# Optimization experiments

Hardware: AMD Instinct MI355X
Metric: run time of the kernel (lower is better)

Reference implementation:

```python
import jax, jax.numpy as jnp
import numpy as np

EPS = 1e-3  # keras LayerNormalization default epsilon

def layernorm(x, gamma, beta):
    mu = jnp.mean(x, axis=-1, keepdims=True)
    var = jnp.var(x, axis=-1, keepdims=True)
    return (x - mu) * jax.lax.rsqrt(var + EPS) * gamma + beta

def setup_inputs() -> dict:
    key = jax.random.key(0)
    ks = jax.random.split(key, 20)
    B, N, T, Dimg, H = 512, 100, 14, 2048, 768
    s = lambda k, *sh: jax.random.normal(k, sh, dtype=jnp.float32) * 0.02
    return {
        "img_feat": jax.random.normal(ks[0], (B, N, Dimg), dtype=jnp.float32),
        "ques_feat": jax.random.normal(ks[1], (B, T, H), dtype=jnp.float32),
        "Wc": s(ks[2], Dimg, H), "bc": jnp.zeros((H,), jnp.float32),
        "Wq": s(ks[3], H, H),    "bq": jnp.zeros((H,), jnp.float32),
        "Wi": s(ks[4], Dimg, H), "bi": jnp.zeros((H,), jnp.float32),
        "wqa": s(ks[5], H, 1), "bqa": jnp.zeros((1,), jnp.float32),
        "wia": s(ks[6], H, 1), "bia": jnp.zeros((1,), jnp.float32),
        "g1": jnp.ones((N,), jnp.float32), "b1": jnp.zeros((N,), jnp.float32),
        "g2": jnp.ones((H,), jnp.float32), "b2": jnp.zeros((H,), jnp.float32),
        "g3": jnp.ones((T,), jnp.float32), "b3": jnp.zeros((T,), jnp.float32),
        "g4": jnp.ones((H,), jnp.float32), "b4": jnp.zeros((H,), jnp.float32),
        "g5": jnp.ones((N,), jnp.float32), "b5": jnp.zeros((N,), jnp.float32),
    }

def reference(img_feat, ques_feat, Wc, bc, Wq, bq, Wi, bi, wqa, bqa, wia, bia,
              g1, b1, g2, b2, g3, b3, g4, b4, g5, b5):
    # img_feat: [B,N,Dimg], ques_feat: [B,T,H]
    img_corr = img_feat @ Wc + bc                                   # [B,N,H]
    wm = jnp.einsum('bth,bnh->btn', ques_feat, img_corr)            # [B,T,N]
    wm = jax.nn.relu(layernorm(wm, g1, b1))
    ques_embed = ques_feat @ Wq + bq                                # [B,T,H]
    img_embed = img_feat @ Wi + bi                                  # [B,N,H]
    transform_img = jnp.einsum('btn,bnh->bth', wm, img_embed)       # [B,T,H]
    ques_atten_sum = jax.nn.relu(layernorm(transform_img + ques_embed, g2, b2))
    # dropout is identity at inference
    ques_atten = (ques_atten_sum @ wqa + bqa)[..., 0]               # [B,T]
    ques_atten = jax.nn.softmax(layernorm(ques_atten, g3, b3), axis=-1)
    transform_ques = jnp.einsum('btn,bth->bnh', wm, ques_embed)     # [B,N,H]
    img_atten_sum = jax.nn.relu(layernorm(transform_ques + img_embed, g4, b4))
    img_atten = (img_atten_sum @ wia + bia)[..., 0]                 # [B,N]
    img_atten = jax.nn.softmax(layernorm(img_atten, g5, b5), axis=-1)
    ques_atten_feat = jnp.einsum('bt,bth->bh', ques_atten, ques_feat)  # [B,H]
    img_atten_feat = jnp.einsum('bn,bnd->bd', img_atten, img_feat)     # [B,Dimg]
    return (img_atten_feat, ques_atten_feat)
```

## Files before the change

### kernel.cpp

```cpp
#include <hip/hip_runtime.h>

using f32x4     = __attribute__((ext_vector_type(4))) float;
using bf16x8    = __attribute__((ext_vector_type(8))) short;
using ushort4_t = __attribute__((ext_vector_type(4))) unsigned short;
using ushort8_t = __attribute__((ext_vector_type(8))) unsigned short;
using uint4_t   = __attribute__((ext_vector_type(4))) unsigned int;

__device__ __forceinline__ unsigned short f2bf(float f) {
    unsigned u = __builtin_bit_cast(unsigned, f);
    u += 0x7fffu + ((u >> 16) & 1u);
    return (unsigned short)(u >> 16);
}
__device__ __forceinline__ float bf2f(unsigned short h) {
    return __builtin_bit_cast(float, (unsigned)h << 16);
}

__device__ __forceinline__ float wave_sum(float v) {
#pragma unroll
    for (int off = 32; off > 0; off >>= 1) v += __shfl_xor(v, off, 64);
    return v;
}
__device__ __forceinline__ float wave_max(float v) {
#pragma unroll
    for (int off = 32; off > 0; off >>= 1) v = fmaxf(v, __shfl_xor(v, off, 64));
    return v;
}

#define GLP(p)  ((const __attribute__((address_space(1))) void*)(p))
#define LDSP(p) ((__attribute__((address_space(3))) void*)(p))

__global__ __launch_bounds__(256) void cvt_bf16(const float* __restrict__ in,
                                                unsigned short* __restrict__ out, long n8) {
    long i = (long)blockIdx.x * 256 + threadIdx.x;
    long stride = (long)gridDim.x * 256;
    for (; i < n8; i += stride) {
        const float4* p = (const float4*)(in + i * 8);
        float4 a = p[0], b = p[1];
        ushort8_t v;
        v[0] = f2bf(a.x); v[1] = f2bf(a.y); v[2] = f2bf(a.z); v[3] = f2bf(a.w);
        v[4] = f2bf(b.x); v[5] = f2bf(b.y); v[6] = f2bf(b.z); v[7] = f2bf(b.w);
        *(ushort8_t*)(out + i * 8) = v;
    }
}

__global__ void pack_w(const float* __restrict__ Wc, const float* __restrict__ Wi,
                       unsigned short* __restrict__ Wp) {
    int n = blockIdx.x, k = blockIdx.y * 256 + threadIdx.x;
    float v = (n < 768) ? Wc[(size_t)k * 768 + n] : Wi[(size_t)k * 768 + (n - 768)];
    Wp[(size_t)n * 2048 + k] = f2bf(v);
}

__global__ void pack_wq(const float* __restrict__ Wq, unsigned short* __restrict__ Wqt) {
    int n = blockIdx.x, k = blockIdx.y * 256 + threadIdx.x;
    Wqt[(size_t)n * 768 + k] = f2bf(Wq[(size_t)k * 768 + n]);
}

template <int OUTBF>
__global__ __launch_bounds__(512, 1) void gemm8(
    const unsigned short* __restrict__ A, const unsigned short* __restrict__ Bt,
    const float* __restrict__ bias0, const float* __restrict__ bias1, int nsplit,
    void* __restrict__ Cv, int N, int K, int NTN)
{
    __shared__ unsigned short LA[4][8192];
    __shared__ unsigned short LB[4][8192];
    const int tid = threadIdx.x, lane = tid & 63, wid = tid >> 6;

    int nwg = (int)gridDim.x, bid = (int)blockIdx.x;
    if ((nwg & 7) == 0) { int cpx = nwg >> 3; bid = (bid & 7) * cpx + (bid >> 3); }
    const int tn = bid % NTN, tm = bid / NTN;
    const size_t m0 = (size_t)tm * 256, n0 = (size_t)tn * 256;
    const int NT = K >> 5;

    const int wr = wid >> 2, wc = wid & 3;
    const int wm = wr * 128, wn = wc * 64;
    const int fr = lane & 15, fs = lane >> 4;

    const int c0 = tid, c1 = tid + 512;
    const int r0 = c0 >> 2, s0 = ((c0 & 3) - (r0 >> 1)) & 3;
    const int r1 = c1 >> 2, s1 = ((c1 & 3) - (r1 >> 1)) & 3;
    const unsigned short* gA0 = A + (m0 + r0) * K + s0 * 8;
    const unsigned short* gA1 = A + (m0 + r1) * K + s1 * 8;
    const unsigned short* gB0 = Bt + (n0 + r0) * K + s0 * 8;
    const unsigned short* gB1 = Bt + (n0 + r1) * K + s1 * 8;

    int offA[8], offB[4];
#pragma unroll
    for (int mf = 0; mf < 8; ++mf) {
        int r = wm + mf * 16 + fr;
        offA[mf] = (4 * r + ((fs + (r >> 1)) & 3)) * 8;
    }
#pragma unroll
    for (int nf = 0; nf < 4; ++nf) {
        int r = wn + nf * 16 + fr;
        offB[nf] = (4 * r + ((fs + (r >> 1)) & 3)) * 8;
    }

    f32x4 acc[8][4];
#pragma unroll
    for (int i = 0; i < 8; ++i)
#pragma unroll
        for (int j = 0; j < 4; ++j) acc[i][j] = (f32x4){0.f, 0.f, 0.f, 0.f};

#pragma unroll
    for (int t = 0; t < 3; ++t) {
        if (t < NT) {
            __builtin_amdgcn_global_load_lds(GLP(gA0 + t * 32), LDSP(&LA[t][c0 * 8]), 16, 0, 0);
            __builtin_amdgcn_global_load_lds(GLP(gA1 + t * 32), LDSP(&LA[t][c1 * 8]), 16, 0, 0);
            __builtin_amdgcn_global_load_lds(GLP(gB0 + t * 32), LDSP(&LB[t][c0 * 8]), 16, 0, 0);
            __builtin_amdgcn_global_load_lds(GLP(gB1 + t * 32), LDSP(&LB[t][c1 * 8]), 16, 0, 0);
        }
    }

    for (int T = 0; T < NT; ++T) {
        const int buf = T & 3, pb = (T + 3) & 3;
        const int rem = NT - 1 - T;
        if (rem >= 2)      asm volatile("s_waitcnt vmcnt(8)" ::: "memory");
        else if (rem == 1) asm volatile("s_waitcnt vmcnt(4)" ::: "memory");
        else               asm volatile("s_waitcnt vmcnt(0)" ::: "memory");
        __builtin_amdgcn_s_barrier();
        __builtin_amdgcn_sched_barrier(0);

        bf16x8 av[4], bv[4];
#pragma unroll
        for (int mf = 0; mf < 4; ++mf) av[mf] = *(const bf16x8*)&LA[buf][offA[mf]];
#pragma unroll
        for (int nf = 0; nf < 4; ++nf) bv[nf] = *(const bf16x8*)&LB[buf][offB[nf]];
        if (T + 3 < NT) {
            __builtin_amdgcn_global_load_lds(GLP(gA0 + (size_t)(T + 3) * 32), LDSP(&LA[pb][c0 * 8]), 16, 0, 0);
            __builtin_amdgcn_global_load_lds(GLP(gA1 + (size_t)(T + 3) * 32), LDSP(&LA[pb][c1 * 8]), 16, 0, 0);
        }
        asm volatile("s_waitcnt lgkmcnt(0)" ::: "memory");
        __builtin_amdgcn_sched_barrier(0);
        __builtin_amdgcn_s_setprio(1);
#pragma unroll
        for (int mf = 0; mf < 4; ++mf)
#pragma unroll
            for (int nf = 0; nf < 4; ++nf)
                acc[mf][nf] = __builtin_amdgcn_mfma_f32_16x16x32_bf16(av[mf], bv[nf], acc[mf][nf], 0, 0, 0);
        __builtin_amdgcn_s_setprio(0);

#pragma unroll
        for (int mf = 0; mf < 4; ++mf) av[mf] = *(const bf16x8*)&LA[buf][offA[4 + mf]];
        if (T + 3 < NT) {
            __builtin_amdgcn_global_load_lds(GLP(gB0 + (size_t)(T + 3) * 32), LDSP(&LB[pb][c0 * 8]), 16, 0, 0);
            __builtin_amdgcn_global_load_lds(GLP(gB1 + (size_t)(T + 3) * 32), LDSP(&LB[pb][c1 * 8]), 16, 0, 0);
        }
        asm volatile("s_waitcnt lgkmcnt(0)" ::: "memory");
        __builtin_amdgcn_sched_barrier(0);
        __builtin_amdgcn_s_setprio(1);
#pragma unroll
        for (int mf = 0; mf < 4; ++mf)
#pragma unroll
            for (int nf = 0; nf < 4; ++nf)
                acc[4 + mf][nf] = __builtin_amdgcn_mfma_f32_16x16x32_bf16(av[mf], bv[nf], acc[4 + mf][nf], 0, 0, 0);
        __builtin_amdgcn_s_setprio(0);
    }

#pragma unroll
    for (int nf = 0; nf < 4; ++nf) {
        int col = (int)n0 + wn + nf * 16 + fr;
        float bs = (col < nsplit) ? bias0[col] : bias1[col - nsplit];
#pragma unroll
        for (int mf = 0; mf < 8; ++mf) {
            size_t rowb = m0 + wm + mf * 16 + fs * 4;
#pragma unroll
            for (int r = 0; r < 4; ++r) {
                float v = acc[mf][nf][r] + bs;
                if (OUTBF) ((unsigned short*)Cv)[(rowb + r) * N + col] = f2bf(v);
                else       ((float*)Cv)[(rowb + r) * N + col] = v;
            }
        }
    }
}

__global__ __launch_bounds__(256) void wm_kernel(
    const unsigned short* __restrict__ qbf, const unsigned short* __restrict__ imgCE,
    const float* __restrict__ g1, const float* __restrict__ b1,
    float* __restrict__ wm_g)
{
    const int b = blockIdx.x, tid = threadIdx.x, lane = tid & 63, wid = tid >> 6;
    __shared__ float qf[14 * 768];
    __shared__ float wmr[14][100];

    const ushort8_t* src = (const ushort8_t*)(qbf + (size_t)b * 14 * 768);
    for (int i = tid; i < 14 * 768 / 8; i += 256) {
        ushort8_t v = src[i];
#pragma unroll
        for (int j = 0; j < 8; ++j) qf[i * 8 + j] = bf2f(v[j]);
    }
    __syncthreads();

    for (int n = wid; n < 100; n += 4) {
        const unsigned short* row = imgCE + ((size_t)b * 100 + n) * 1536;
        float r[12];
#pragma unroll
        for (int j = 0; j < 12; ++j) r[j] = bf2f(row[lane + 64 * j]);
        for (int t = 0; t < 14; ++t) {
            const float* q = qf + t * 768;
            float s = 0.f;
#pragma unroll
            for (int j = 0; j < 12; ++j) s = fmaf(r[j], q[lane + 64 * j], s);
            s = wave_sum(s);
            if (lane == 0) wmr[t][n] = s;
        }
    }
    __syncthreads();

    for (int t = wid; t < 14; t += 4) {
        float x0 = wmr[t][lane];
        float x1 = (lane + 64 < 100) ? wmr[t][lane + 64] : 0.f;
        float s = wave_sum(x0 + x1);
        float q = wave_sum(x0 * x0 + x1 * x1);
        float mu = s * (1.f / 100.f);
        float var = q * (1.f / 100.f) - mu * mu;
        float rs = rsqrtf(var + 1e-3f);
        float* dst = wm_g + ((size_t)b * 14 + t) * 100;
        {
            float v = (x0 - mu) * rs * g1[lane] + b1[lane];
            dst[lane] = v > 0.f ? v : 0.f;
        }
        if (lane + 64 < 100) {
            float v = (x1 - mu) * rs * g1[lane + 64] + b1[lane + 64];
            dst[lane + 64] = v > 0.f ? v : 0.f;
        }
    }
}

__global__ __launch_bounds__(256) void ques_kernel(
    const float* __restrict__ qf_g, const float* __restrict__ qe_g,
    const unsigned short* __restrict__ imgCE, const float* __restrict__ wm_g,
    const float* __restrict__ g2, const float* __restrict__ b2,
    const float* __restrict__ g3, const float* __restrict__ b3,
    const float* __restrict__ wqa, const float* __restrict__ bqa,
    float* __restrict__ out_q)
{
    const int b = blockIdx.x, tid = threadIdx.x, lane = tid & 63, wid = tid >> 6;
    __shared__ float qe[14 * 768];
    __shared__ float wm[14 * 100];
    __shared__ float red[4][28];
    __shared__ float mu_s[14], rs_s[14], qa_s[14], qw_s[14];

    {
        const float4* src = (const float4*)(qe_g + (size_t)b * 14 * 768);
        for (int i = tid; i < 14 * 768 / 4; i += 256) ((float4*)qe)[i] = src[i];
        const float* ws = wm_g + (size_t)b * 1400;
        for (int i = tid; i < 1400; i += 256) wm[i] = ws[i];
    }
    __syncthreads();

    float a0[14], a1[14], a2[14];
#pragma unroll
    for (int t = 0; t < 14; ++t) { a0[t] = 0.f; a1[t] = 0.f; a2[t] = 0.f; }

    const unsigned short* ie_base = imgCE + (size_t)b * 100 * 1536 + 768;
    for (int n = 0; n < 100; ++n) {
        const unsigned short* ie = ie_base + (size_t)n * 1536;
        float e0 = bf2f(ie[tid]), e1 = bf2f(ie[tid + 256]), e2 = bf2f(ie[tid + 512]);
#pragma unroll
        for (int t = 0; t < 14; ++t) {
            float w = wm[t * 100 + n];
            a0[t] = fmaf(w, e0, a0[t]); a1[t] = fmaf(w, e1, a1[t]); a2[t] = fmaf(w, e2, a2[t]);
        }
    }
#pragma unroll
    for (int t = 0; t < 14; ++t) {
        a0[t] += qe[t * 768 + tid];
        a1[t] += qe[t * 768 + tid + 256];
        a2[t] += qe[t * 768 + tid + 512];
    }
#pragma unroll
    for (int t = 0; t < 14; ++t) {
        float s = wave_sum(a0[t] + a1[t] + a2[t]);
        float q = wave_sum(a0[t] * a0[t] + a1[t] * a1[t] + a2[t] * a2[t]);
        if (lane == 0) { red[wid][t] = s; red[wid][14 + t] = q; }
    }
    __syncthreads();
    if (tid < 14) {
        float s = red[0][tid] + red[1][tid] + red[2][tid] + red[3][tid];
        float q = red[0][14 + tid] + red[1][14 + tid] + red[2][14 + tid] + red[3][14 + tid];
        float mu = s * (1.f / 768.f);
        float var = q * (1.f / 768.f) - mu * mu;
        mu_s[tid] = mu; rs_s[tid] = rsqrtf(var + 1e-3f);
    }
    __syncthreads();

    float ga = g2[tid], ba = b2[tid], gb = g2[tid + 256], bb = b2[tid + 256],
          gc = g2[tid + 512], bc_ = b2[tid + 512];
    float w0 = wqa[tid], w1 = wqa[tid + 256], w2 = wqa[tid + 512];
#pragma unroll
    for (int t = 0; t < 14; ++t) {
        float mu = mu_s[t], rs = rs_s[t];
        float v0 = fmaxf((a0[t] - mu) * rs * ga + ba, 0.f);
        float v1 = fmaxf((a1[t] - mu) * rs * gb + bb, 0.f);
        float v2 = fmaxf((a2[t] - mu) * rs * gc + bc_, 0.f);
        float p = wave_sum(v0 * w0 + v1 * w1 + v2 * w2);
        if (lane == 0) red[wid][t] = p;
    }
    __syncthreads();
    if (tid < 14) qa_s[tid] = red[0][tid] + red[1][tid] + red[2][tid] + red[3][tid] + bqa[0];
    __syncthreads();
    if (tid == 0) {
        float s = 0.f;
        for (int t = 0; t < 14; ++t) s += qa_s[t];
        float mu = s * (1.f / 14.f);
        float q = 0.f;
        for (int t = 0; t < 14; ++t) { float d = qa_s[t] - mu; q += d * d; }
        float rs = rsqrtf(q * (1.f / 14.f) + 1e-3f);
        float e[14], mx = -1e30f;
        for (int t = 0; t < 14; ++t) { e[t] = (qa_s[t] - mu) * rs * g3[t] + b3[t]; mx = fmaxf(mx, e[t]); }
        float se = 0.f;
        for (int t = 0; t < 14; ++t) { e[t] = expf(e[t] - mx); se += e[t]; }
        float inv = 1.f / se;
        for (int t = 0; t < 14; ++t) qw_s[t] = e[t] * inv;
    }
    __syncthreads();

    const float* qf = qf_g + (size_t)b * 14 * 768;
#pragma unroll
    for (int c = 0; c < 3; ++c) {
        int h = tid + c * 256;
        float o = 0.f;
#pragma unroll
        for (int t = 0; t < 14; ++t) o = fmaf(qw_s[t], qf[t * 768 + h], o);
        out_q[(size_t)b * 768 + h] = o;
    }
}

__global__ __launch_bounds__(256) void img_kernel(
    const unsigned short* __restrict__ imf_bf, const float* __restrict__ qe_g,
    const unsigned short* __restrict__ imgCE, const float* __restrict__ wm_g,
    const float* __restrict__ g4, const float* __restrict__ b4,
    const float* __restrict__ g5, const float* __restrict__ b5,
    const float* __restrict__ wia, const float* __restrict__ bia,
    float* __restrict__ out_i)
{
    const int b = blockIdx.x, tid = threadIdx.x, lane = tid & 63, wid = tid >> 6;
    __shared__ float qe[14 * 768];
    __shared__ float wm[14 * 100];
    __shared__ float red[4][20];
    __shared__ float mu_s[10], rs_s[10];
    __shared__ float ia_s[100], iw_s[100];

    {
        const float4* src = (const float4*)(qe_g + (size_t)b * 14 * 768);
        for (int i = tid; i < 14 * 768 / 4; i += 256) ((float4*)qe)[i] = src[i];
        const float* ws = wm_g + (size_t)b * 1400;
        for (int i = tid; i < 1400; i += 256) wm[i] = ws[i];
    }
    __syncthreads();

    float g4a = g4[tid], b4a = b4[tid], g4b = g4[tid + 256], b4b = b4[tid + 256],
          g4c = g4[tid + 512], b4c = b4[tid + 512];
    float wa = wia[tid], wb = wia[tid + 256], wc_ = wia[tid + 512];

    for (int g = 0; g < 10; ++g) {
        float t0[10], t1[10], t2[10];
#pragma unroll
        for (int i = 0; i < 10; ++i) { t0[i] = 0.f; t1[i] = 0.f; t2[i] = 0.f; }
#pragma unroll
        for (int t = 0; t < 14; ++t) {
            float q0 = qe[t * 768 + tid], q1 = qe[t * 768 + tid + 256], q2 = qe[t * 768 + tid + 512];
#pragma unroll
            for (int i = 0; i < 10; ++i) {
                float w = wm[t * 100 + g * 10 + i];
                t0[i] = fmaf(w, q0, t0[i]); t1[i] = fmaf(w, q1, t1[i]); t2[i] = fmaf(w, q2, t2[i]);
            }
        }
#pragma unroll
        for (int i = 0; i < 10; ++i) {
            const unsigned short* ie = imgCE + ((size_t)b * 100 + g * 10 + i) * 1536 + 768;
            t0[i] += bf2f(ie[tid]); t1[i] += bf2f(ie[tid + 256]); t2[i] += bf2f(ie[tid + 512]);
            float s = wave_sum(t0[i] + t1[i] + t2[i]);
            float q = wave_sum(t0[i] * t0[i] + t1[i] * t1[i] + t2[i] * t2[i]);
            if (lane == 0) { red[wid][i] = s; red[wid][10 + i] = q; }
        }
        __syncthreads();
        if (tid < 10) {
            float s = red[0][tid] + red[1][tid] + red[2][tid] + red[3][tid];
            float q = red[0][10 + tid] + red[1][10 + tid] + red[2][10 + tid] + red[3][10 + tid];
            float mu = s * (1.f / 768.f);
            float var = q * (1.f / 768.f) - mu * mu;
            mu_s[tid] = mu; rs_s[tid] = rsqrtf(var + 1e-3f);
        }
        __syncthreads();
#pragma unroll
        for (int i = 0; i < 10; ++i) {
            float mu = mu_s[i], rs = rs_s[i];
            float v0 = fmaxf((t0[i] - mu) * rs * g4a + b4a, 0.f);
            float v1 = fmaxf((t1[i] - mu) * rs * g4b + b4b, 0.f);
            float v2 = fmaxf((t2[i] - mu) * rs * g4c + b4c, 0.f);
            float p = wave_sum(v0 * wa + v1 * wb + v2 * wc_);
            if (lane == 0) red[wid][i] = p;
        }
        __syncthreads();
        if (tid < 10) ia_s[g * 10 + tid] = red[0][tid] + red[1][tid] + red[2][tid] + red[3][tid] + bia[0];
        __syncthreads();
    }

    if (wid == 0) {
        float x0 = ia_s[lane];
        float x1 = (lane + 64 < 100) ? ia_s[lane + 64] : 0.f;
        float s = wave_sum(x0 + x1);
        float q = wave_sum(x0 * x0 + x1 * x1);
        float mu = s * 0.01f;
        float var = q * 0.01f - mu * mu;
        float rs = rsqrtf(var + 1e-3f);
        float v0 = (x0 - mu) * rs * g5[lane] + b5[lane];
        float v1 = (lane + 64 < 100) ? (x1 - mu) * rs * g5[lane + 64] + b5[lane + 64] : -1e30f;
        float mx = wave_max(fmaxf(v0, v1));
        float e0 = expf(v0 - mx);
        float e1 = (lane + 64 < 100) ? expf(v1 - mx) : 0.f;
        float se = wave_sum(e0 + e1);
        float inv = 1.f / se;
        iw_s[lane] = e0 * inv;
        if (lane + 64 < 100) iw_s[lane + 64] = e1 * inv;
    }
    __syncthreads();

    const unsigned short* imf = imf_bf + (size_t)b * 100 * 2048;
    float acc8[8];
#pragma unroll
    for (int j = 0; j < 8; ++j) acc8[j] = 0.f;
    for (int n = 0; n < 100; ++n) {
        ushort8_t v = *(const ushort8_t*)(imf + (size_t)n * 2048 + tid * 8);
        float w = iw_s[n];
#pragma unroll
        for (int j = 0; j < 8; ++j) acc8[j] = fmaf(w, bf2f(v[j]), acc8[j]);
    }
    float4* dst = (float4*)(out_i + (size_t)b * 2048);
    float4 oA = {acc8[0], acc8[1], acc8[2], acc8[3]};
    float4 oB = {acc8[4], acc8[5], acc8[6], acc8[7]};
    dst[tid * 2] = oA; dst[tid * 2 + 1] = oB;
}

extern "C" void kernel_launch(void* const* d_in, const int* in_sizes, int n_in,
                              void* d_out, int out_size, void* d_ws, size_t ws_size,
                              hipStream_t stream)
{
    const float* img_feat = (const float*)d_in[0];
    const float* ques_feat = (const float*)d_in[1];
    const float* Wc = (const float*)d_in[2];
    const float* bc = (const float*)d_in[3];
    const float* Wq = (const float*)d_in[4];
    const float* bq = (const float*)d_in[5];
    const float* Wi = (const float*)d_in[6];
    const float* bi = (const float*)d_in[7];
    const float* wqa = (const float*)d_in[8];
    const float* bqa = (const float*)d_in[9];
    const float* wia = (const float*)d_in[10];
    const float* bia = (const float*)d_in[11];
    const float* g1 = (const float*)d_in[12]; const float* b1 = (const float*)d_in[13];
    const float* g2 = (const float*)d_in[14]; const float* b2 = (const float*)d_in[15];
    const float* g3 = (const float*)d_in[16]; const float* b3 = (const float*)d_in[17];
    const float* g4 = (const float*)d_in[18]; const float* b4 = (const float*)d_in[19];
    const float* g5 = (const float*)d_in[20]; const float* b5 = (const float*)d_in[21];

    const size_t SZ_WP   = 1536u * 2048u * 2u;
    const size_t SZ_WQT  = 768u * 768u * 2u;
    const size_t SZ_IMG  = 51200ull * 1536u * 2u;
    const size_t SZ_QE   = 7168u * 768u * 4u;
    const size_t SZ_WM   = 512u * 1400u * 4u;
    const size_t SZ_ABF  = 51200ull * 2048u * 2u;
    const size_t SZ_QBF  = 7168u * 768u * 2u;

    const size_t OFF_WP  = 0;
    const size_t OFF_WQT = OFF_WP + SZ_WP;
    const size_t OFF_IMG = OFF_WQT + SZ_WQT;
    const size_t OFF_QE  = OFF_IMG + SZ_IMG;
    const size_t OFF_WM  = OFF_QE + SZ_QE;
    const size_t OFF_ABF = OFF_WM + SZ_WM;
    const size_t OFF_QBF = OFF_ABF + SZ_ABF;
    const size_t NEED    = OFF_QBF + SZ_QBF;
    if (ws_size < NEED) return;

    char* ws = (char*)d_ws;
    unsigned short* Wp    = (unsigned short*)(ws + OFF_WP);
    unsigned short* Wqt   = (unsigned short*)(ws + OFF_WQT);
    unsigned short* imgCE = (unsigned short*)(ws + OFF_IMG);
    float*          qe    = (float*)(ws + OFF_QE);
    float*          wm    = (float*)(ws + OFF_WM);
    unsigned short* Abf   = (unsigned short*)(ws + OFF_ABF);
    unsigned short* Qbf   = (unsigned short*)(ws + OFF_QBF);

    float* out_img = (float*)d_out;
    float* out_q   = (float*)d_out + 512 * 2048;

    hipLaunchKernelGGL(pack_w,  dim3(1536, 8), dim3(256), 0, stream, Wc, Wi, Wp);
    hipLaunchKernelGGL(pack_wq, dim3(768, 3),  dim3(256), 0, stream, Wq, Wqt);
    hipLaunchKernelGGL(cvt_bf16, dim3(2048), dim3(256), 0, stream,
                       img_feat, Abf, (long)(51200ull * 2048u / 8u));
    hipLaunchKernelGGL(cvt_bf16, dim3(1024), dim3(256), 0, stream,
                       ques_feat, Qbf, (long)(7168u * 768u / 8u));

    hipLaunchKernelGGL(HIP_KERNEL_NAME(gemm8<1>), dim3(1200), dim3(512), 0, stream,
                       Abf, Wp, bc, bi, 768, (void*)imgCE, 1536, 2048, 6);
    hipLaunchKernelGGL(HIP_KERNEL_NAME(gemm8<0>), dim3(84), dim3(512), 0, stream,
                       Qbf, Wqt, bq, bq, 768, (void*)qe, 768, 768, 3);

    hipLaunchKernelGGL(wm_kernel, dim3(512), dim3(256), 0, stream,
                       Qbf, imgCE, g1, b1, wm);
    hipLaunchKernelGGL(ques_kernel, dim3(512), dim3(256), 0, stream,
                       ques_feat, qe, imgCE, wm, g2, b2, g3, b3, wqa, bqa, out_q);
    hipLaunchKernelGGL(img_kernel, dim3(512), dim3(256), 0, stream,
                       Abf, qe, imgCE, wm, g4, b4, g5, b5, wia, bia, out_img);
}
```

Measured before the change: 810.0 us.

## Restructure GEMM mainloop to 64-wide K tiles with 8-phase ping-pong schedule

The bf16 MFMA GEMM main loop now uses K-tiles of 64 instead of 32, held in two double-buffered LDS stages split into two 128-row halves per operand. Each iteration covers two K-tiles in eight sub-phases that interleave LDS fragment reads, global-to-LDS prefetches and MFMA quadrants, with barriers and priority hints between them. The XOR swizzle changes to an 8-chunk pattern. The goal is fewer barriers per unit of K and better overlap of loads with matrix math, in exchange for many more barriers per iteration, a more complex schedule, and the assumption that K is a multiple of 128.

After: 798.8 us. About the same (-1.4%).

```diff
diff --git a/kernel.cpp b/kernel.cpp
--- a/kernel.cpp
+++ b/kernel.cpp
@@ -2,9 +2,7 @@
 
 using f32x4     = __attribute__((ext_vector_type(4))) float;
 using bf16x8    = __attribute__((ext_vector_type(8))) short;
-using ushort4_t = __attribute__((ext_vector_type(4))) unsigned short;
 using ushort8_t = __attribute__((ext_vector_type(8))) unsigned short;
-using uint4_t   = __attribute__((ext_vector_type(4))) unsigned int;
 
 __device__ __forceinline__ unsigned short f2bf(float f) {
     unsigned u = __builtin_bit_cast(unsigned, f);
@@ -61,101 +59,159 @@
     const float* __restrict__ bias0, const float* __restrict__ bias1, int nsplit,
     void* __restrict__ Cv, int N, int K, int NTN)
 {
-    __shared__ unsigned short LA[4][8192];
-    __shared__ unsigned short LB[4][8192];
+    __shared__ unsigned short LA[2][2][8192];
+    __shared__ unsigned short LB[2][2][8192];
     const int tid = threadIdx.x, lane = tid & 63, wid = tid >> 6;
 
     int nwg = (int)gridDim.x, bid = (int)blockIdx.x;
     if ((nwg & 7) == 0) { int cpx = nwg >> 3; bid = (bid & 7) * cpx + (bid >> 3); }
     const int tn = bid % NTN, tm = bid / NTN;
     const size_t m0 = (size_t)tm * 256, n0 = (size_t)tn * 256;
-    const int NT = K >> 5;
+    const int NT = K >> 6;
+    const int NIT = NT >> 1;
 
     const int wr = wid >> 2, wc = wid & 3;
+    const int hb = wc >> 1;
+    const int fr = lane & 15, fs = lane >> 4;
+
+    const int r0 = tid >> 3, s0 = ((tid & 7) - r0) & 7;
+    const int r1 = r0 + 64,  s1 = ((tid & 7) - r1) & 7;
+    const unsigned short* pA[2][2];
+    const unsigned short* pB[2][2];
+#pragma unroll
+    for (int h = 0; h < 2; ++h) {
+        pA[h][0] = A  + (m0 + h * 128 + r0) * K + s0 * 8;
+        pA[h][1] = A  + (m0 + h * 128 + r1) * K + s1 * 8;
+        pB[h][0] = Bt + (n0 + h * 128 + r0) * K + s0 * 8;
+        pB[h][1] = Bt + (n0 + h * 128 + r1) * K + s1 * 8;
+    }
+    const int d0 = tid * 8, d1 = (tid + 512) * 8;
+
+#define STG_A(h, t, B_) do { \
+    __builtin_amdgcn_global_load_lds(GLP(pA[h][0] + (size_t)(t) * 64), LDSP(&LA[B_][h][d0]), 16, 0, 0); \
+    __builtin_amdgcn_global_load_lds(GLP(pA[h][1] + (size_t)(t) * 64), LDSP(&LA[B_][h][d1]), 16, 0, 0); \
+} while (0)
+#define STG_B(h, t, B_) do { \
+    __builtin_amdgcn_global_load_lds(GLP(pB[h][0] + (size_t)(t) * 64), LDSP(&LB[B_][h][d0]), 16, 0, 0); \
+    __builtin_amdgcn_global_load_lds(GLP(pB[h][1] + (size_t)(t) * 64), LDSP(&LB[B_][h][d1]), 16, 0, 0); \
+} while (0)
+
+    int offA[2][4], offB[2][2];
+#pragma unroll
+    for (int mq = 0; mq < 2; ++mq)
+#pragma unroll
+        for (int mfl = 0; mfl < 4; ++mfl) {
+            int r = mq * 64 + mfl * 16 + fr;
+            offA[mq][mfl] = r * 64 + ((fs + r) & 7) * 8;
+        }
+#pragma unroll
+    for (int nq = 0; nq < 2; ++nq)
+#pragma unroll
+        for (int nfl = 0; nfl < 2; ++nfl) {
+            int r = (wc & 1) * 64 + nq * 32 + nfl * 16 + fr;
+            offB[nq][nfl] = r * 64 + ((fs + r) & 7) * 8;
+        }
+
+#define LDA_SUB(B_, mq) do { \
+    _Pragma("unroll") \
+    for (int mfl = 0; mfl < 4; ++mfl) { \
+        av[mfl][0] = *(const bf16x8*)&LA[B_][wr][offA[mq][mfl]]; \
+        av[mfl][1] = *(const bf16x8*)&LA[B_][wr][offA[mq][mfl] ^ 32]; \
+    } } while (0)
+#define LDB_SUB(B_, nq, bv) do { \
+    _Pragma("unroll") \
+    for (int nfl = 0; nfl < 2; ++nfl) { \
+        bv[nfl][0] = *(const bf16x8*)&LB[B_][hb][offB[nq][nfl]]; \
+        bv[nfl][1] = *(const bf16x8*)&LB[B_][hb][offB[nq][nfl] ^ 32]; \
+    } } while (0)
+#define MMA_Q(mq, nq, bv) do { \
+    _Pragma("unroll") \
+    for (int ks = 0; ks < 2; ++ks) \
+    _Pragma("unroll") \
+    for (int mfl = 0; mfl < 4; ++mfl) \
+    _Pragma("unroll") \
+    for (int nfl = 0; nfl < 2; ++nfl) \
+        acc[mq * 4 + mfl][nq * 2 + nfl] = __builtin_amdgcn_mfma_f32_16x16x32_bf16( \
+            av[mfl][ks], bv[nfl][ks], acc[mq * 4 + mfl][nq * 2 + nfl], 0, 0, 0); \
+    } while (0)
+#define BAR  __builtin_amdgcn_s_barrier()
+#define SCB  __builtin_amdgcn_sched_barrier(0)
+#define LGKM0 do { asm volatile("s_waitcnt lgkmcnt(0)" ::: "memory"); SCB; } while (0)
+#define PRIO1 __builtin_amdgcn_s_setprio(1)
+#define PRIO0 __builtin_amdgcn_s_setprio(0)
+
+    f32x4 acc[8][4];
+#pragma unroll
+    for (int i = 0; i < 8; ++i)
+#pragma unroll
+        for (int j = 0; j < 4; ++j) acc[i][j] = (f32x4){0.f, 0.f, 0.f, 0.f};
+
+    STG_A(0, 0, 0); STG_A(1, 0, 0); STG_B(0, 0, 0); STG_B(1, 0, 0);
+    STG_B(0, 1, 1); STG_B(1, 1, 1);
+    asm volatile("s_waitcnt vmcnt(4)" ::: "memory");
+    SCB; BAR;
+
+    for (int i = 0; i < NIT; ++i) {
+        const int t0 = 2 * i, t1 = 2 * i + 1;
+        const bool st = (t0 + 2 < NT);
+        bf16x8 av[4][2], bv0[2][2], bv1[2][2];
+
+        LDA_SUB(0, 0); LDB_SUB(0, 0, bv0);
+        STG_A(0, t1, 1);
+        SCB; BAR; LGKM0;
+        PRIO1; MMA_Q(0, 0, bv0); PRIO0;
+        BAR;
+        LDB_SUB(0, 1, bv1);
+        STG_A(1, t1, 1);
+        SCB; BAR; LGKM0;
+        PRIO1; MMA_Q(0, 1, bv1); PRIO0;
+        BAR;
+        LDA_SUB(0, 1);
+        if (st) STG_B(0, t0 + 2, 0);
+        SCB; BAR; LGKM0;
+        PRIO1; MMA_Q(1, 1, bv1); PRIO0;
+        BAR;
+        if (st) STG_B(1, t0 + 2, 0);
+        SCB; BAR;
+        PRIO1; MMA_Q(1, 0, bv0); PRIO0;
+        if (st) asm volatile("s_waitcnt vmcnt(4)" ::: "memory");
+        else    asm volatile("s_waitcnt vmcnt(0)" ::: "memory");
+        SCB; BAR;
+        LDA_SUB(1, 0); LDB_SUB(1, 0, bv0);
+        if (st) STG_A(0, t0 + 2, 0);
+        SCB; BAR; LGKM0;
+        PRIO1; MMA_Q(0, 0, bv0); PRIO0;
+        BAR;
+        LDB_SUB(1, 1, bv1);
+        if (st) STG_A(1, t0 + 2, 0);
+        SCB; BAR; LGKM0;
+        PRIO1; MMA_Q(0, 1, bv1); PRIO0;
+        BAR;
+        LDA_SUB(1, 1);
+        if (st) STG_B(0, t1 + 2, 1);
+        SCB; BAR; LGKM0;
+        PRIO1; MMA_Q(1, 1, bv1); PRIO0;
+        BAR;
+        if (st) STG_B(1, t1 + 2, 1);
+        SCB; BAR;
+        PRIO1; MMA_Q(1, 0, bv0); PRIO0;
+        if (st) asm volatile("s_waitcnt vmcnt(4)" ::: "memory");
+        else    asm volatile("s_waitcnt vmcnt(0)" ::: "memory");
+        SCB; BAR;
+    }
+
+#undef STG_A
+#undef STG_B
+#undef LDA_SUB
+#undef LDB_SUB
+#undef MMA_Q
+#undef BAR
+#undef SCB
+#undef LGKM0
+#undef PRIO1
+#undef PRIO0
+
     const int wm = wr * 128, wn = wc * 64;
-    const int fr = lane & 15, fs = lane >> 4;
-
-    const int c0 = tid, c1 = tid + 512;
-    const int r0 = c0 >> 2, s0 = ((c0 & 3) - (r0 >> 1)) & 3;
-    const int r1 = c1 >> 2, s1 = ((c1 & 3) - (r1 >> 1)) & 3;
-    const unsigned short* gA0 = A + (m0 + r0) * K + s0 * 8;
-    const unsigned short* gA1 = A + (m0 + r1) * K + s1 * 8;
-    const unsigned short* gB0 = Bt + (n0 + r0) * K + s0 * 8;
-    const unsigned short* gB1 = Bt + (n0 + r1) * K + s1 * 8;
-
-    int offA[8], offB[4];
-#pragma unroll
-    for (int mf = 0; mf < 8; ++mf) {
-        int r = wm + mf * 16 + fr;
-        offA[mf] = (4 * r + ((fs + (r >> 1)) & 3)) * 8;
-    }
-#pragma unroll
-    for (int nf = 0; nf < 4; ++nf) {
-        int r = wn + nf * 16 + fr;
-        offB[nf] = (4 * r + ((fs + (r >> 1)) & 3)) * 8;
-    }
-
-    f32x4 acc[8][4];
-#pragma unroll
-    for (int i = 0; i < 8; ++i)
-#pragma unroll
-        for (int j = 0; j < 4; ++j) acc[i][j] = (f32x4){0.f, 0.f, 0.f, 0.f};
-
-#pragma unroll
-    for (int t = 0; t < 3; ++t) {
-        if (t < NT) {
-            __builtin_amdgcn_global_load_lds(GLP(gA0 + t * 32), LDSP(&LA[t][c0 * 8]), 16, 0, 0);
-            __builtin_amdgcn_global_load_lds(GLP(gA1 + t * 32), LDSP(&LA[t][c1 * 8]), 16, 0, 0);
-            __builtin_amdgcn_global_load_lds(GLP(gB0 + t * 32), LDSP(&LB[t][c0 * 8]), 16, 0, 0);
-            __builtin_amdgcn_global_load_lds(GLP(gB1 + t * 32), LDSP(&LB[t][c1 * 8]), 16, 0, 0);
-        }
-    }
-
-    for (int T = 0; T < NT; ++T) {
-        const int buf = T & 3, pb = (T + 3) & 3;
-        const int rem = NT - 1 - T;
-        if (rem >= 2)      asm volatile("s_waitcnt vmcnt(8)" ::: "memory");
-        else if (rem == 1) asm volatile("s_waitcnt vmcnt(4)" ::: "memory");
-        else               asm volatile("s_waitcnt vmcnt(0)" ::: "memory");
-        __builtin_amdgcn_s_barrier();
-        __builtin_amdgcn_sched_barrier(0);
-
-        bf16x8 av[4], bv[4];
-#pragma unroll
-        for (int mf = 0; mf < 4; ++mf) av[mf] = *(const bf16x8*)&LA[buf][offA[mf]];
-#pragma unroll
-        for (int nf = 0; nf < 4; ++nf) bv[nf] = *(const bf16x8*)&LB[buf][offB[nf]];
-        if (T + 3 < NT) {
-            __builtin_amdgcn_global_load_lds(GLP(gA0 + (size_t)(T + 3) * 32), LDSP(&LA[pb][c0 * 8]), 16, 0, 0);
-            __builtin_amdgcn_global_load_lds(GLP(gA1 + (size_t)(T + 3) * 32), LDSP(&LA[pb][c1 * 8]), 16, 0, 0);
-        }
-        asm volatile("s_waitcnt lgkmcnt(0)" ::: "memory");
-        __builtin_amdgcn_sched_barrier(0);
-        __builtin_amdgcn_s_setprio(1);
-#pragma unroll
-        for (int mf = 0; mf < 4; ++mf)
-#pragma unroll
-            for (int nf = 0; nf < 4; ++nf)
-                acc[mf][nf] = __builtin_amdgcn_mfma_f32_16x16x32_bf16(av[mf], bv[nf], acc[mf][nf], 0, 0, 0);
-        __builtin_amdgcn_s_setprio(0);
-
-#pragma unroll
-        for (int mf = 0; mf < 4; ++mf) av[mf] = *(const bf16x8*)&LA[buf][offA[4 + mf]];
-        if (T + 3 < NT) {
-            __builtin_amdgcn_global_load_lds(GLP(gB0 + (size_t)(T + 3) * 32), LDSP(&LB[pb][c0 * 8]), 16, 0, 0);
-            __builtin_amdgcn_global_load_lds(GLP(gB1 + (size_t)(T + 3) * 32), LDSP(&LB[pb][c1 * 8]), 16, 0, 0);
-        }
-        asm volatile("s_waitcnt lgkmcnt(0)" ::: "memory");
-        __builtin_amdgcn_sched_barrier(0);
-        __builtin_amdgcn_s_setprio(1);
-#pragma unroll
-        for (int mf = 0; mf < 4; ++mf)
-#pragma unroll
-            for (int nf = 0; nf < 4; ++nf)
-                acc[4 + mf][nf] = __builtin_amdgcn_mfma_f32_16x16x32_bf16(av[mf], bv[nf], acc[4 + mf][nf], 0, 0, 0);
-        __builtin_amdgcn_s_setprio(0);
-    }
-
 #pragma unroll
     for (int nf = 0; nf < 4; ++nf) {
         int col = (int)n0 + wn + nf * 16 + fr;
```
